# Optimization experiments

Hardware: AMD Instinct MI355X
Metric: run time of the kernel (lower is better)

The kernel has to match this reference:

```python
import jax, jax.numpy as jnp
import numpy as np

N_BATCH = 2; N_RAYS = 4096; S_COARSE = 32; S_FINE = 32
FEATURE_DIM = 32; BOX_WARP = 6.0; EPS = 1e-5

_PLANE_AXES = np.array([[[1, 0, 0], [0, 1, 0], [0, 0, 1]],
                        [[1, 0, 0], [0, 0, 1], [0, 1, 0]],
                        [[0, 0, 1], [0, 1, 0], [1, 0, 0]]], dtype=np.float32)
_INV_PLANES = np.linalg.inv(_PLANE_AXES)  # [3,3,3]


def _grid_sample(feat, coords):
    # feat [B,C,H,W], coords [B,M,2] in [-1,1] (x->W, y->H); bilinear, align_corners=False, zero padding
    B, C, H, W = feat.shape
    x = (coords[..., 0] + 1.0) * (W * 0.5) - 0.5
    y = (coords[..., 1] + 1.0) * (H * 0.5) - 0.5
    x0 = jnp.floor(x); y0 = jnp.floor(y)
    wx = x - x0; wy = y - y0
    x0i = x0.astype(jnp.int32); y0i = y0.astype(jnp.int32)

    def corner(fb, yi, xi):
        valid = ((xi >= 0) & (xi < W) & (yi >= 0) & (yi < H)).astype(fb.dtype)
        v = fb[:, jnp.clip(yi, 0, H - 1), jnp.clip(xi, 0, W - 1)]  # [C,M]
        return v * valid[None, :]

    def one(fb, x0b, y0b, wxb, wyb):
        x1b = x0b + 1; y1b = y0b + 1
        return (corner(fb, y0b, x0b) * (1 - wxb) * (1 - wyb)
                + corner(fb, y0b, x1b) * wxb * (1 - wyb)
                + corner(fb, y1b, x0b) * (1 - wxb) * wyb
                + corner(fb, y1b, x1b) * wxb * wyb)  # [C,M]

    return jax.vmap(one)(feat, x0i, y0i, wx, wy)  # [B,C,M]


def _sample_from_planes(planes, coords):
    # planes [N,3,C,H,W], coords [N,M,3] -> [N,3,M,C]
    N, n_planes, C, H, W = planes.shape
    M = coords.shape[1]
    c = coords * (2.0 / BOX_WARP)
    proj = jnp.einsum('nmc,pcd->npmd', c, jnp.asarray(_INV_PLANES))[..., :2]  # [N,3,M,2]
    out = _grid_sample(planes.reshape(N * n_planes, C, H, W), proj.reshape(N * n_planes, M, 2))
    return out.reshape(N, n_planes, C, M).transpose(0, 1, 3, 2)


def _decoder(feat, W1, b1, W2, b2):
    # OSGDecoder: Linear -> softplus -> Linear; rgb sigmoid-squashed, sigma raw
    h = jax.nn.softplus(feat @ W1 + b1)
    o = h @ W2 + b2
    rgb = jax.nn.sigmoid(o[..., 1:]) * (1 + 2 * 0.001) - 0.001
    sigma = o[..., 0:1]
    return rgb, sigma


def _run_model(planes, coords, W1, b1, W2, b2, beta):
    sf = _sample_from_planes(planes, coords).mean(axis=1)  # [N,M,C]
    rgb, raw_sigma = _decoder(sf, W1, b1, W2, b2)
    pred_sdf = raw_sigma
    # template SDF stand-in (external FLAME tex_feature net): sphere SDF
    tsdf = jnp.linalg.norm(coords, axis=-1, keepdims=True) - 0.5
    sigma = raw_sigma + tsdf
    density = jax.nn.sigmoid(-sigma / beta) / beta  # sdf_activation(-sigma)
    return rgb, density, pred_sdf


def _ray_march(colors, densities, depths):
    deltas = depths[:, :, 1:] - depths[:, :, :-1]
    c_mid = 0.5 * (colors[:, :, :-1] + colors[:, :, 1:])
    d_mid = 0.5 * (densities[:, :, :-1] + densities[:, :, 1:])
    z_mid = 0.5 * (depths[:, :, :-1] + depths[:, :, 1:])
    alpha = 1.0 - jnp.exp(-d_mid * deltas)
    shifted = jnp.concatenate([jnp.ones_like(alpha[:, :, :1]), 1.0 - alpha + 1e-10], axis=2)
    weights = alpha * jnp.cumprod(shifted, axis=2)[:, :, :-1]
    comp_rgb = jnp.sum(weights * c_mid, axis=2) * 2.0 - 1.0
    w_tot = jnp.sum(weights, axis=2)
    comp_depth = jnp.sum(weights * z_mid, axis=2) / w_tot
    comp_depth = jnp.nan_to_num(comp_depth, nan=jnp.inf)
    comp_depth = jnp.clip(comp_depth, depths.min(), depths.max())
    return comp_rgb, comp_depth, weights


def _sample_pdf(bins, weights, u):
    n_w = weights.shape[-1]
    w = weights + EPS
    pdf = w / jnp.sum(w, axis=-1, keepdims=True)
    cdf = jnp.cumsum(pdf, axis=-1)
    cdf = jnp.concatenate([jnp.zeros_like(cdf[:, :1]), cdf], axis=-1)
    inds = jax.vmap(lambda c, uu: jnp.searchsorted(c, uu, side='right'))(cdf, u)
    below = jnp.maximum(inds - 1, 0)
    above = jnp.minimum(inds, n_w)
    cdf0 = jnp.take_along_axis(cdf, below, axis=-1)
    cdf1 = jnp.take_along_axis(cdf, above, axis=-1)
    b0 = jnp.take_along_axis(bins, below, axis=-1)
    b1v = jnp.take_along_axis(bins, above, axis=-1)
    denom = cdf1 - cdf0
    denom = jnp.where(denom < EPS, 1.0, denom)
    return b0 + (u - cdf0) / denom * (b1v - b0)


def _sample_importance(z_vals, weights, u):
    B, R, S, _ = z_vals.shape
    z = z_vals.reshape(B * R, S)
    w = weights.reshape(B * R, -1)  # S-1
    # torch max_pool1d(k=2,s=1,pad=1) then avg_pool1d(k=2,s=1)
    neg = jnp.full_like(w[:, :1], -1e10)
    wp = jnp.concatenate([neg, w, neg], axis=-1)
    m = jnp.maximum(wp[:, :-1], wp[:, 1:])  # len S
    w_sm = 0.5 * (m[:, :-1] + m[:, 1:]) + 0.01  # len S-1
    z_mid = 0.5 * (z[:, :-1] + z[:, 1:])  # len S-1
    s = _sample_pdf(z_mid, w_sm[:, 1:-1], u)
    return jax.lax.stop_gradient(s.reshape(B, R, -1, 1))


def reference(planes, ray_origins, ray_directions, hit_min_depth, hit_max_depth, jitter, u_importance, W1, b1, W2, b2, sigmoid_beta, hit_mask):
    N, M, _ = ray_origins.shape
    beta = jnp.maximum(sigmoid_beta, 0.002)
    mask = hit_mask.astype(planes.dtype)[:, :, None, None]  # [N,M,1,1]
    hmin = jnp.where(mask == 0, hit_min_depth.min(), hit_min_depth)
    hmax = jnp.where(mask == 0, hit_max_depth.max(), hit_max_depth)
    base = jnp.linspace(0.0, 1.0, S_COARSE, dtype=planes.dtype).reshape(1, 1, S_COARSE, 1)
    span = hmax - hmin
    d_coarse = (base + jitter * span / S_COARSE) * span + hmin  # [N,M,S,1]

    def eval_points(depths):
        coords = ray_origins[:, :, None, :] + depths * ray_directions[:, :, None, :]
        S = depths.shape[2]
        rgb, dens, psdf = _run_model(planes, coords.reshape(N, M * S, 3), W1, b1, W2, b2, beta)
        # masked scatter-back into dense buffers == multiply by hit mask
        rgb = rgb.reshape(N, M, S, FEATURE_DIM) * mask
        dens = dens.reshape(N, M, S, 1) * mask
        return rgb, dens, psdf

    rgb_c, dens_c, psdf_c = eval_points(d_coarse)
    _, _, w_c = _ray_march(rgb_c, dens_c, d_coarse)
    d_fine = _sample_importance(d_coarse, w_c, u_importance)
    rgb_f, dens_f, psdf_f = eval_points(d_fine)

    all_d = jnp.concatenate([d_coarse, d_fine], axis=2)
    all_c = jnp.concatenate([rgb_c, rgb_f], axis=2)
    all_s = jnp.concatenate([dens_c, dens_f], axis=2)
    idx = jnp.argsort(all_d, axis=2)
    all_d = jnp.take_along_axis(all_d, idx, axis=2)
    all_c = jnp.take_along_axis(all_c, jnp.broadcast_to(idx, all_c.shape), axis=2)
    all_s = jnp.take_along_axis(all_s, jnp.broadcast_to(idx, all_s.shape), axis=2)

    rgb_final, depth_final, weights = _ray_march(all_c, all_s, all_d)
    all_pred_sdf = jnp.concatenate([psdf_c, psdf_f], axis=1)
    return rgb_final, depth_final, weights, all_pred_sdf


def setup_inputs():
    key = jax.random.key(0)
    ks = jax.random.split(key, 12)
    planes = jax.random.normal(ks[0], (N_BATCH, 3, 32, 256, 256), jnp.float32)
    ray_origins = 0.1 * jax.random.normal(ks[1], (N_BATCH, N_RAYS, 3), jnp.float32)
    rd = jax.random.normal(ks[2], (N_BATCH, N_RAYS, 3), jnp.float32)
    ray_directions = rd / jnp.linalg.norm(rd, axis=-1, keepdims=True)
    hit_min_depth = 0.8 + 0.4 * jax.random.uniform(ks[3], (N_BATCH, N_RAYS, 1, 1), jnp.float32)
    hit_max_depth = hit_min_depth + 0.5 + jax.random.uniform(ks[4], (N_BATCH, N_RAYS, 1, 1), jnp.float32)
    jitter = jax.random.uniform(ks[5], (N_BATCH, N_RAYS, S_COARSE, 1), jnp.float32)
    u_importance = jax.random.uniform(ks[6], (N_BATCH * N_RAYS, S_FINE), jnp.float32)
    W1 = 0.05 * jax.random.normal(ks[7], (32, 64), jnp.float32)
    b1 = jnp.zeros((64,), jnp.float32)
    W2 = 0.05 * jax.random.normal(ks[8], (64, 1 + FEATURE_DIM), jnp.float32)
    b2 = jnp.zeros((1 + FEATURE_DIM,), jnp.float32)
    sigmoid_beta = 0.1 * jnp.ones((1,), jnp.float32)
    hit_mask = jax.random.randint(ks[9], (N_BATCH, N_RAYS), 0, 2, jnp.int32)
    return {'planes': planes, 'ray_origins': ray_origins, 'ray_directions': ray_directions,
            'hit_min_depth': hit_min_depth, 'hit_max_depth': hit_max_depth, 'jitter': jitter,
            'u_importance': u_importance, 'W1': W1, 'b1': b1, 'W2': W2, 'b2': b2,
            'sigmoid_beta': sigmoid_beta, 'hit_mask': hit_mask}
```

## Files before the change

kernel.cpp:

```cpp
#include <hip/hip_runtime.h>
#include <hip/hip_bf16.h>
#include <math.h>
#include <stddef.h>

typedef unsigned int u32;
typedef unsigned short u16;
typedef unsigned long long u64;

#define NRAYS 8192
#define NSAMP 262144

__device__ __forceinline__ float fa(float a,float b){ return __fadd_rn(a,b); }
__device__ __forceinline__ float fs(float a,float b){ return __fsub_rn(a,b); }
__device__ __forceinline__ float fm(float a,float b){ return __fmul_rn(a,b); }
__device__ __forceinline__ float fdv(float a,float b){ return __fdiv_rn(a,b); }

__device__ __forceinline__ double exp_d(double x){
  const double LOG2E  = 1.4426950408889634074;
  const double LN2_HI = 6.93147180369123816490e-01;
  const double LN2_LO = 1.90821492927058770002e-10;
  double kd = rint(x * LOG2E);
  if (kd >  200.0) return INFINITY;
  if (kd < -200.0) return 0.0;
  int k = (int)kd;
  double r = fma(-kd, LN2_HI, x);
  r = fma(-kd, LN2_LO, r);
  double p = 1.0/39916800.0;
  p = fma(p, r, 1.0/3628800.0);
  p = fma(p, r, 1.0/362880.0);
  p = fma(p, r, 1.0/40320.0);
  p = fma(p, r, 1.0/5040.0);
  p = fma(p, r, 1.0/720.0);
  p = fma(p, r, 1.0/120.0);
  p = fma(p, r, 1.0/24.0);
  p = fma(p, r, 1.0/6.0);
  p = fma(p, r, 0.5);
  p = fma(p, r, 1.0);
  p = fma(p, r, 1.0);
  u64 sb = ((u64)(k + 1023)) << 52;
  return p * __longlong_as_double((long long)sb);
}
__device__ __forceinline__ float exf(float x){ return (float)exp_d((double)x); }
__device__ __forceinline__ float sigm(float x){
  if (x >= 0.f){ float e = exf(-x); return fdv(1.f, fa(1.f, e)); }
  float e = exf(x); return fdv(e, fa(1.f, e));
}
__device__ __forceinline__ float sigm_fast(float x){
  return 1.f/(1.f + __expf(-x));
}
__device__ __forceinline__ u16 f2b(float f){
  u32 x = __float_as_uint(f);
  return (u16)((x + 0x7fffu + ((x>>16)&1u)) >> 16);
}
__device__ __forceinline__ u32 fenc(float f){ u32 b=__float_as_uint(f); return (b&0x80000000u)? ~b : (b|0x80000000u); }
__device__ __forceinline__ float fdec(u32 k){ u32 b=(k&0x80000000u)? (k^0x80000000u) : ~k; return __uint_as_float(b); }

__global__ void k_init(const float* __restrict__ hmin, const float* __restrict__ hmax,
                       const float* __restrict__ W1, float* __restrict__ scal,
                       float* __restrict__ W1t){
  __shared__ float smn[256], smx[256];
  int t = threadIdx.x;
  float mn = 1e30f, mx = -1e30f;
  for (int i=t;i<NRAYS;i+=256){ mn=fminf(mn,hmin[i]); mx=fmaxf(mx,hmax[i]); }
  smn[t]=mn; smx[t]=mx; __syncthreads();
  for(int s=128;s>0;s>>=1){
    if(t<s){ smn[t]=fminf(smn[t],smn[t+s]); smx[t]=fmaxf(smx[t],smx[t+s]); }
    __syncthreads();
  }
  if(t==0){
    scal[0]=smn[0]; scal[1]=smx[0];
    ((u32*)scal)[2]=0xFFFFFFFFu;
    ((u32*)scal)[3]=0u;
  }
  for(int i=t;i<2048;i+=256){ int j=i>>5, c=i&31; W1t[i]=W1[c*64+j]; }
}

__global__ void __launch_bounds__(256) k_tr(const float* __restrict__ pl, float* __restrict__ pt){
  int t = blockIdx.x*256 + threadIdx.x;
  int x  = t & 255;
  int c4 = ((t>>8)&7)<<2;
  int y  = (t>>11)&255;
  int np = t>>19;
  const float* ip = pl + (((size_t)(np*32+c4))<<16) + (y<<8) + x;
  float4 o;
  o.x = ip[0];
  o.y = ip[65536];
  o.z = ip[131072];
  o.w = ip[196608];
  *reinterpret_cast<float4*>(pt + ((((size_t)(np<<8|y))<<8|x)<<5) + c4) = o;
}

template<int PHASE>
__global__ void __launch_bounds__(256) k_eval(
  const float* __restrict__ pt, const float* __restrict__ ro, const float* __restrict__ rd,
  const float* __restrict__ hmin, const float* __restrict__ hmax,
  const float* __restrict__ jitter, const int* __restrict__ hitmask,
  const float* __restrict__ W1t, const float* __restrict__ b1,
  const float* __restrict__ W2, const float* __restrict__ b2,
  const float* __restrict__ sb, float* __restrict__ scal,
  float* __restrict__ dep, float* __restrict__ dens_out, u16* __restrict__ rgb_out,
  float* __restrict__ out_psdf)
{
  int idx = blockIdx.x*256 + threadIdx.x;
  int ray = idx >> 5;
  int s   = idx & 31;
  int n   = ray >> 12;
  int msk = hitmask[ray];

  float d;
  if (PHASE==0){
    float hmn = msk ? hmin[ray] : scal[0];
    float hmx = msk ? hmax[ray] : scal[1];
    float span = fs(hmx, hmn);
    float jit  = jitter[idx];
    float base = (float)((double)s * (1.0/31.0));
    if (s==31) base = 1.0f;
    float t1 = fdv(fm(jit, span), 32.0f);
    d = fa(fm(fa(base, t1), span), hmn);
    dep[idx] = d;
    float dm=d, dM=d;
#pragma unroll
    for (int m=1;m<64;m<<=1){ dm=fminf(dm,__shfl_xor(dm,m)); dM=fmaxf(dM,__shfl_xor(dM,m)); }
    if ((threadIdx.x & 63)==0){
      atomicMin(((u32*)scal)+2, fenc(dm));
      atomicMax(((u32*)scal)+3, fenc(dM));
    }
  } else {
    d = dep[idx];
  }

  float ox=ro[ray*3+0], oy=ro[ray*3+1], oz=ro[ray*3+2];
  float dx=rd[ray*3+0], dy=rd[ray*3+1], dz=rd[ray*3+2];
  float px = fa(ox, fm(d,dx)), py = fa(oy, fm(d,dy)), pz = fa(oz, fm(d,dz));
  float nrm = __fsqrt_rn(fa(fa(fm(px,px),fm(py,py)),fm(pz,pz)));
  float tsdf = fs(nrm, 0.5f);
  const float sc2 = (float)(2.0/6.0);
  float cx=fm(px,sc2), cy=fm(py,sc2), cz=fm(pz,sc2);

  float feat[32];
#pragma unroll
  for(int c=0;c<32;c++) feat[c]=0.f;

#pragma unroll
  for (int p=0;p<3;p++){
    float u = (p==2)?cz:cx;
    float v = (p==1)?cz:cy;
    float fx = fs(fm(fa(u,1.f),128.f),0.5f);
    float fy = fs(fm(fa(v,1.f),128.f),0.5f);
    float x0f = floorf(fx), y0f = floorf(fy);
    float wx = fs(fx,x0f), wy = fs(fy,y0f);
    float ax0 = fs(1.f,wx), ax1 = wx, ay0 = fs(1.f,wy), ay1 = wy;
    int x0, y0;
    {
      x0 = (x0f >= 2.1e9f) ? 2147483647 : ((x0f <= -2.1e9f) ? (-2147483647-1) : (int)x0f);
      y0 = (y0f >= 2.1e9f) ? 2147483647 : ((y0f <= -2.1e9f) ? (-2147483647-1) : (int)y0f);
    }
    int x1=x0+1, y1=y0+1;
    bool vx0 = (x0>=0 && x0<256), vx1 = (x1>=0 && x1<256);
    bool vy0 = (y0>=0 && y0<256), vy1 = (y1>=0 && y1<256);
    bool ok00 = vx0&&vy0, ok01 = vx1&&vy0, ok10 = vx0&&vy1, ok11 = vx1&&vy1;
    int cx0=min(max(x0,0),255), cx1=min(max(x1,0),255);
    int cy0=min(max(y0,0),255), cy1=min(max(y1,0),255);
    int npl = n*3+p;
    size_t pb = ((size_t)npl)<<16;
    const float4* t00 = (const float4*)(pt + ((pb + (cy0<<8) + cx0)<<5));
    const float4* t01 = (const float4*)(pt + ((pb + (cy0<<8) + cx1)<<5));
    const float4* t10 = (const float4*)(pt + ((pb + (cy1<<8) + cx0)<<5));
    const float4* t11 = (const float4*)(pt + ((pb + (cy1<<8) + cx1)<<5));
#pragma unroll
    for(int q=0;q<8;q++){
      float4 v00 = t00[q], v01 = t01[q], v10 = t10[q], v11 = t11[q];
      float e0,e1,e2,e3, t_;
#define CORNER_SUM(FLD, OUTI) \
      e0 = ok00 ? v00.FLD : 0.f; e1 = ok01 ? v01.FLD : 0.f; \
      e2 = ok10 ? v10.FLD : 0.f; e3 = ok11 ? v11.FLD : 0.f; \
      t_ = fa(fa(fa(fm(fm(e0,ax0),ay0), fm(fm(e1,ax1),ay0)), fm(fm(e2,ax0),ay1)), fm(fm(e3,ax1),ay1)); \
      feat[q*4+OUTI] = fa(feat[q*4+OUTI], t_);
      CORNER_SUM(x,0) CORNER_SUM(y,1) CORNER_SUM(z,2) CORNER_SUM(w,3)
#undef CORNER_SUM
    }
  }
#pragma unroll
  for(int c=0;c<32;c++) feat[c] = fdv(feat[c], 3.0f);

  float o[33];
#pragma unroll
  for(int k=0;k<33;k++) o[k]=0.f;
#pragma unroll 2
  for(int j=0;j<64;j++){
    float a = 0.f;
#pragma unroll
    for(int c=0;c<32;c++) a = fmaf(feat[c], W1t[j*32+c], a);
    a = fa(a, b1[j]);
    float h = fa(fmaxf(a,0.f), __logf(fa(1.f, __expf(-fabsf(a)))));
#pragma unroll
    for(int k=0;k<33;k++) o[k] = fmaf(h, W2[j*33+k], o[k]);
  }
#pragma unroll
  for(int k=0;k<33;k++) o[k] = fa(o[k], b2[k]);

  float beta = fmaxf(sb[0], 0.002f);
  float raw = o[0];
  out_psdf[((size_t)n<<18) + ((size_t)PHASE<<17) + (size_t)(ray&4095)*32 + s] = raw;
  float sg = fa(raw, tsdf);
  float dens = msk ? fdv(sigm(fdv(-sg, beta)), beta) : 0.f;
  dens_out[idx]=dens;

  u16 rv[32];
#pragma unroll
  for(int c=0;c<32;c++){
    float r = msk ? fs(fm(sigm_fast(o[c+1]), 1.002f), 0.001f) : 0.f;
    rv[c]=f2b(r);
  }
  uint4* op = (uint4*)(rgb_out + (size_t)idx*32);
#pragma unroll
  for(int q=0;q<4;q++){
    uint4 w;
    w.x = (u32)rv[q*8+0] | ((u32)rv[q*8+1]<<16);
    w.y = (u32)rv[q*8+2] | ((u32)rv[q*8+3]<<16);
    w.z = (u32)rv[q*8+4] | ((u32)rv[q*8+5]<<16);
    w.w = (u32)rv[q*8+6] | ((u32)rv[q*8+7]<<16);
    op[q]=w;
  }
}

__global__ void __launch_bounds__(64) k_imp(
  const float* __restrict__ dc, const float* __restrict__ dens,
  const float* __restrict__ u_imp, float* __restrict__ df, float* __restrict__ scal)
{
  __shared__ float scdf[64][30];
  __shared__ float szm [64][30];
  int tid = threadIdx.x;
  int ray = blockIdx.x*64 + tid;
  float w[31];
  float dprev = dc[ray*32+0];
  float sprev = dens[ray*32+0];
  float T = 1.f;
#pragma unroll
  for(int i=0;i<31;i++){
    float dn = dc[ray*32+i+1];
    float sn = dens[ray*32+i+1];
    if (i<30) szm[tid][i] = fm(0.5f, fa(dprev,dn));
    float delta = fs(dn,dprev);
    float dm = fm(0.5f, fa(sprev,sn));
    float al = fs(1.f, exf(-fm(dm,delta)));
    w[i] = fm(al,T);
    T = fm(T, fa(fs(1.f,al), 1e-10f));
    dprev=dn; sprev=sn;
  }
  float pdfw[29];
#pragma unroll
  for(int i=0;i<29;i++){
    float m1 = fmaxf(w[i],w[i+1]), m2 = fmaxf(w[i+1],w[i+2]);
    pdfw[i] = fa(fa(fm(0.5f, fa(m1,m2)), 0.01f), 1e-5f);
  }
  float sum;
  {
    float r[8];
#pragma unroll
    for(int j=0;j<8;j++) r[j]=pdfw[j];
#pragma unroll
    for(int j=0;j<8;j++) r[j]=fa(r[j],pdfw[8+j]);
#pragma unroll
    for(int j=0;j<8;j++) r[j]=fa(r[j],pdfw[16+j]);
    sum = fa(fa(fa(r[0],r[1]),fa(r[2],r[3])), fa(fa(r[4],r[5]),fa(r[6],r[7])));
#pragma unroll
    for(int i=24;i<29;i++) sum = fa(sum, pdfw[i]);
  }
  {
    float cacc = 0.f;
    scdf[tid][0] = 0.f;
#pragma unroll
    for(int i=1;i<30;i++){
      cacc = fa(cacc, fdv(pdfw[i-1], sum));
      scdf[tid][i] = cacc;
    }
  }

  float fmn=1e30f, fmx=-1e30f;
  for(int k=0;k<32;k++){
    float u = u_imp[ray*32+k];
    int lo=0, hi=30;
    while(lo<hi){
      int mid=(lo+hi)>>1;
      if (scdf[tid][mid] <= u) lo = mid+1; else hi = mid;
    }
    int ind = lo;
    int below = ind-1;
    int above = (ind>29)?29:ind;
    float cdf0 = scdf[tid][below];
    float cdf1 = scdf[tid][above];
    float b0   = szm [tid][below];
    float b1v  = szm [tid][above];
    float den = fs(cdf1,cdf0);
    if((double)den < 1e-5) den = 1.f;
    float sres = fa(b0, fm(fdv(fs(u,cdf0),den), fs(b1v,b0)));
    df[ray*32+k]=sres;
    fmn=fminf(fmn,sres); fmx=fmaxf(fmx,sres);
  }
#pragma unroll
  for(int m=1;m<64;m<<=1){ fmn=fminf(fmn,__shfl_xor(fmn,m)); fmx=fmaxf(fmx,__shfl_xor(fmx,m)); }
  if(tid==0){
    atomicMin(((u32*)scal)+2, fenc(fmn));
    atomicMax(((u32*)scal)+3, fenc(fmx));
  }
}

__global__ void __launch_bounds__(256) k_final(
  const float* __restrict__ dc, const float* __restrict__ df,
  const float* __restrict__ densc, const float* __restrict__ densf,
  const u16* __restrict__ rgbc, const u16* __restrict__ rgbf,
  const float* __restrict__ scal,
  float* __restrict__ out_rgb, float* __restrict__ out_depth, float* __restrict__ out_w)
{
  __shared__ float ssd[4][64];
  __shared__ float ssn[4][64];
  __shared__ int   sp [4][64];
  __shared__ float swv[4][64];
  __shared__ float swz[4][64];
  int wid = threadIdx.x>>6, lane = threadIdx.x&63;
  int ray = blockIdx.x*4 + wid;

  float myd = (lane<32)? dc[ray*32+lane]    : df[ray*32+lane-32];
  float myn = (lane<32)? densc[ray*32+lane] : densf[ray*32+lane-32];
  ssd[wid][lane]=myd; __syncthreads();
  int rk=0;
#pragma unroll 8
  for(int j=0;j<64;j++){
    float dj = ssd[wid][j];
    rk += (dj<myd || (dj==myd && j<lane)) ? 1:0;
  }
  __syncthreads();
  ssd[wid][rk]=myd; ssn[wid][rk]=myn; sp[wid][rk]=lane;
  __syncthreads();

  float T=1.f, accr=0.f;
  int j0 = sp[wid][0];
  float cprev = 0.f;
  if (lane<32){
    const u16* cb = (j0<32)? (rgbc+((size_t)ray*32+j0)*32) : (rgbf+((size_t)ray*32+(j0-32))*32);
    cprev = __uint_as_float(((u32)cb[lane])<<16);
  }
  float d0 = ssd[wid][0], n0 = ssn[wid][0];
  for(int s2=0;s2<63;s2++){
    float d1 = ssd[wid][s2+1], n1 = ssn[wid][s2+1];
    float delta = fs(d1,d0);
    float dm = fm(0.5f, fa(n0,n1));
    float al = fs(1.f, exf(-fm(dm,delta)));
    float wv = fm(al,T);
    T = fm(T, fa(fs(1.f,al), 1e-10f));
    if (lane==s2){ swv[wid][s2]=wv; swz[wid][s2]=fm(wv, fm(0.5f, fa(d0,d1))); }
    int j1 = sp[wid][s2+1];
    float cnext = 0.f;
    if (lane<32){
      const u16* cb = (j1<32)? (rgbc+((size_t)ray*32+j1)*32) : (rgbf+((size_t)ray*32+(j1-32))*32);
      cnext = __uint_as_float(((u32)cb[lane])<<16);
    }
    accr = fa(accr, fm(wv, fm(0.5f, fa(cprev,cnext))));
    cprev=cnext; d0=d1; n0=n1;
  }
  __syncthreads();
  if(lane<63) out_w[(size_t)ray*63+lane]=swv[wid][lane];
  if(lane<32) out_rgb[(size_t)ray*32+lane]=fs(fm(accr,2.f),1.f);
  if(lane==0){
    float wsum, zsum;
    {
      float r[8], rz[8];
#pragma unroll
      for(int j=0;j<8;j++){ r[j]=swv[wid][j]; rz[j]=swz[wid][j]; }
      for(int i=8;i<56;i+=8)
#pragma unroll
        for(int j=0;j<8;j++){ r[j]=fa(r[j],swv[wid][i+j]); rz[j]=fa(rz[j],swz[wid][i+j]); }
      wsum = fa(fa(fa(r[0],r[1]),fa(r[2],r[3])), fa(fa(r[4],r[5]),fa(r[6],r[7])));
      zsum = fa(fa(fa(rz[0],rz[1]),fa(rz[2],rz[3])), fa(fa(rz[4],rz[5]),fa(rz[6],rz[7])));
      for(int i=56;i<63;i++){ wsum=fa(wsum,swv[wid][i]); zsum=fa(zsum,swz[wid][i]); }
    }
    float depv = fdv(zsum, wsum);
    if (isnan(depv)) depv = INFINITY;
    float lo = fdec(((const u32*)scal)[2]);
    float hi = fdec(((const u32*)scal)[3]);
    depv = fminf(fmaxf(depv,lo),hi);
    out_depth[ray]=depv;
  }
}

extern "C" void kernel_launch(void* const* d_in, const int* in_sizes, int n_in,
                              void* d_out, int out_size, void* d_ws, size_t ws_size,
                              hipStream_t stream) {
  const float* planes = (const float*)d_in[0];
  const float* ro     = (const float*)d_in[1];
  const float* rdp    = (const float*)d_in[2];
  const float* hmin   = (const float*)d_in[3];
  const float* hmax   = (const float*)d_in[4];
  const float* jitter = (const float*)d_in[5];
  const float* uimp   = (const float*)d_in[6];
  const float* W1     = (const float*)d_in[7];
  const float* b1     = (const float*)d_in[8];
  const float* W2     = (const float*)d_in[9];
  const float* b2     = (const float*)d_in[10];
  const float* sb     = (const float*)d_in[11];
  const int*   hmk    = (const int*)d_in[12];
  float* out = (float*)d_out;
  char* ws = (char*)d_ws;

  size_t off=0;
  auto alloc=[&](size_t bytes){ size_t o=off; off=(off+bytes+255)&~(size_t)255; return o; };
  float* scal = (float*)(ws+alloc(64));
  float* W1t  = (float*)(ws+alloc(2048*4));
  float* pt   = (float*)(ws+alloc((size_t)12582912*4));
  float* dco  = (float*)(ws+alloc((size_t)NSAMP*4));
  float* dfi  = (float*)(ws+alloc((size_t)NSAMP*4));
  float* dnc  = (float*)(ws+alloc((size_t)NSAMP*4));
  float* dnf  = (float*)(ws+alloc((size_t)NSAMP*4));
  u16*   rgc  = (u16*)  (ws+alloc((size_t)NSAMP*32*2));
  u16*   rgf  = (u16*)  (ws+alloc((size_t)NSAMP*32*2));
  (void)in_sizes; (void)n_in; (void)out_size; (void)ws_size;

  float* out_rgb  = out;
  float* out_dep  = out + 262144;
  float* out_w    = out + 270336;
  float* out_psdf = out + 786432;

  k_init<<<dim3(1),dim3(256),0,stream>>>(hmin,hmax,W1,scal,W1t);
  k_tr<<<dim3(12288),dim3(256),0,stream>>>(planes, pt);
  k_eval<0><<<dim3(1024),dim3(256),0,stream>>>(pt,ro,rdp,hmin,hmax,jitter,hmk,W1t,b1,W2,b2,sb,scal,dco,dnc,rgc,out_psdf);
  k_imp<<<dim3(128),dim3(64),0,stream>>>(dco,dnc,uimp,dfi,scal);
  k_eval<1><<<dim3(1024),dim3(256),0,stream>>>(pt,ro,rdp,hmin,hmax,jitter,hmk,W1t,b1,W2,b2,sb,scal,dfi,dnf,rgf,out_psdf);
  k_final<<<dim3(2048),dim3(256),0,stream>>>(dco,dfi,dnc,dnf,rgc,rgf,scal,out_rgb,out_dep,out_w);
}
```

Measured before the change: 457.5 us.

## Cooperatively gather plane features with 8 lanes per sample via shared memory

The triplane bilinear gather is restructured so that 8 lanes cooperate on each sample point, each loading one float4 channel chunk from the four corners. Results are staged in shared memory and then read back per thread for the MLP. This makes the gather loads coalesced across lanes, where previously each thread fetched 32 contiguous floats on its own. In exchange, sample position is recomputed per chunk, the kernel gains about 33 KB of LDS and a block barrier, and the per-sample gather loop is serialized over 8 rounds.

```diff
diff --git a/kernel.cpp b/kernel.cpp
--- a/kernel.cpp
+++ b/kernel.cpp
@@ -101,7 +101,12 @@
   float* __restrict__ dep, float* __restrict__ dens_out, u16* __restrict__ rgb_out,
   float* __restrict__ out_psdf)
 {
-  int idx = blockIdx.x*256 + threadIdx.x;
+  __shared__ float sfeat[4][64][33];
+  int tid = threadIdx.x;
+  int wid = tid>>6, lane = tid&63;
+  int blockbase = blockIdx.x*256;
+  int wavebase  = blockbase + (wid<<6);
+  int idx = blockbase + tid;
   int ray = idx >> 5;
   int s   = idx & 31;
   int n   = ray >> 12;
@@ -121,7 +126,7 @@
     float dm=d, dM=d;
 #pragma unroll
     for (int m=1;m<64;m<<=1){ dm=fminf(dm,__shfl_xor(dm,m)); dM=fmaxf(dM,__shfl_xor(dM,m)); }
-    if ((threadIdx.x & 63)==0){
+    if ((tid & 63)==0){
       atomicMin(((u32*)scal)+2, fenc(dm));
       atomicMax(((u32*)scal)+3, fenc(dM));
     }
@@ -129,59 +134,93 @@
     d = dep[idx];
   }
 
-  float ox=ro[ray*3+0], oy=ro[ray*3+1], oz=ro[ray*3+2];
-  float dx=rd[ray*3+0], dy=rd[ray*3+1], dz=rd[ray*3+2];
-  float px = fa(ox, fm(d,dx)), py = fa(oy, fm(d,dy)), pz = fa(oz, fm(d,dz));
-  float nrm = __fsqrt_rn(fa(fa(fm(px,px),fm(py,py)),fm(pz,pz)));
-  float tsdf = fs(nrm, 0.5f);
+  float tsdf;
+  {
+    float ox=ro[ray*3+0], oy=ro[ray*3+1], oz=ro[ray*3+2];
+    float dx=rd[ray*3+0], dy=rd[ray*3+1], dz=rd[ray*3+2];
+    float px = fa(ox, fm(d,dx)), py = fa(oy, fm(d,dy)), pz = fa(oz, fm(d,dz));
+    float nrm = __fsqrt_rn(fa(fa(fm(px,px),fm(py,py)),fm(pz,pz)));
+    tsdf = fs(nrm, 0.5f);
+  }
+
   const float sc2 = (float)(2.0/6.0);
-  float cx=fm(px,sc2), cy=fm(py,sc2), cz=fm(pz,sc2);
-
-  float feat[32];
-#pragma unroll
-  for(int c=0;c<32;c++) feat[c]=0.f;
-
-#pragma unroll
-  for (int p=0;p<3;p++){
-    float u = (p==2)?cz:cx;
-    float v = (p==1)?cz:cy;
-    float fx = fs(fm(fa(u,1.f),128.f),0.5f);
-    float fy = fs(fm(fa(v,1.f),128.f),0.5f);
-    float x0f = floorf(fx), y0f = floorf(fy);
-    float wx = fs(fx,x0f), wy = fs(fy,y0f);
-    float ax0 = fs(1.f,wx), ax1 = wx, ay0 = fs(1.f,wy), ay1 = wy;
-    int x0, y0;
-    {
-      x0 = (x0f >= 2.1e9f) ? 2147483647 : ((x0f <= -2.1e9f) ? (-2147483647-1) : (int)x0f);
-      y0 = (y0f >= 2.1e9f) ? 2147483647 : ((y0f <= -2.1e9f) ? (-2147483647-1) : (int)y0f);
-    }
-    int x1=x0+1, y1=y0+1;
-    bool vx0 = (x0>=0 && x0<256), vx1 = (x1>=0 && x1<256);
-    bool vy0 = (y0>=0 && y0<256), vy1 = (y1>=0 && y1<256);
-    bool ok00 = vx0&&vy0, ok01 = vx1&&vy0, ok10 = vx0&&vy1, ok11 = vx1&&vy1;
-    int cx0=min(max(x0,0),255), cx1=min(max(x1,0),255);
-    int cy0=min(max(y0,0),255), cy1=min(max(y1,0),255);
-    int npl = n*3+p;
-    size_t pb = ((size_t)npl)<<16;
-    const float4* t00 = (const float4*)(pt + ((pb + (cy0<<8) + cx0)<<5));
-    const float4* t01 = (const float4*)(pt + ((pb + (cy0<<8) + cx1)<<5));
-    const float4* t10 = (const float4*)(pt + ((pb + (cy1<<8) + cx0)<<5));
-    const float4* t11 = (const float4*)(pt + ((pb + (cy1<<8) + cx1)<<5));
-#pragma unroll
-    for(int q=0;q<8;q++){
-      float4 v00 = t00[q], v01 = t01[q], v10 = t10[q], v11 = t11[q];
+  int pg = lane >> 3;
+  int q  = lane & 7;
+#pragma unroll 1
+  for (int r=0;r<8;r++){
+    int p2   = wavebase + r*8 + pg;
+    int ray2 = p2 >> 5;
+    int s2   = p2 & 31;
+    int n2   = ray2 >> 12;
+    float d2;
+    if (PHASE==0){
+      int msk2 = hitmask[ray2];
+      float hmn = msk2 ? hmin[ray2] : scal[0];
+      float hmx = msk2 ? hmax[ray2] : scal[1];
+      float span = fs(hmx, hmn);
+      float jit  = jitter[p2];
+      float base = (float)((double)s2 * (1.0/31.0));
+      if (s2==31) base = 1.0f;
+      float t1 = fdv(fm(jit, span), 32.0f);
+      d2 = fa(fm(fa(base, t1), span), hmn);
+    } else {
+      d2 = dep[p2];
+    }
+    float ox=ro[ray2*3+0], oy=ro[ray2*3+1], oz=ro[ray2*3+2];
+    float dx=rd[ray2*3+0], dy=rd[ray2*3+1], dz=rd[ray2*3+2];
+    float px = fa(ox, fm(d2,dx)), py = fa(oy, fm(d2,dy)), pz = fa(oz, fm(d2,dz));
+    float cx=fm(px,sc2), cy=fm(py,sc2), cz=fm(pz,sc2);
+
+    float fchunk[4];
+#pragma unroll
+    for(int i=0;i<4;i++) fchunk[i]=0.f;
+
+#pragma unroll
+    for (int p=0;p<3;p++){
+      float u = (p==2)?cz:cx;
+      float v = (p==1)?cz:cy;
+      float fx = fs(fm(fa(u,1.f),128.f),0.5f);
+      float fy = fs(fm(fa(v,1.f),128.f),0.5f);
+      float x0f = floorf(fx), y0f = floorf(fy);
+      float wx = fs(fx,x0f), wy = fs(fy,y0f);
+      float ax0 = fs(1.f,wx), ax1 = wx, ay0 = fs(1.f,wy), ay1 = wy;
+      int x0, y0;
+      {
+        x0 = (x0f >= 2.1e9f) ? 2147483647 : ((x0f <= -2.1e9f) ? (-2147483647-1) : (int)x0f);
+        y0 = (y0f >= 2.1e9f) ? 2147483647 : ((y0f <= -2.1e9f) ? (-2147483647-1) : (int)y0f);
+      }
+      int x1=x0+1, y1=y0+1;
+      bool vx0 = (x0>=0 && x0<256), vx1 = (x1>=0 && x1<256);
+      bool vy0 = (y0>=0 && y0<256), vy1 = (y1>=0 && y1<256);
+      bool ok00 = vx0&&vy0, ok01 = vx1&&vy0, ok10 = vx0&&vy1, ok11 = vx1&&vy1;
+      int cx0=min(max(x0,0),255), cx1=min(max(x1,0),255);
+      int cy0=min(max(y0,0),255), cy1=min(max(y1,0),255);
+      size_t pb = ((size_t)(n2*3+p))<<16;
+      int qo = q<<2;
+      const float4* t00 = (const float4*)(pt + ((pb + (cy0<<8) + cx0)<<5) + qo);
+      const float4* t01 = (const float4*)(pt + ((pb + (cy0<<8) + cx1)<<5) + qo);
+      const float4* t10 = (const float4*)(pt + ((pb + (cy1<<8) + cx0)<<5) + qo);
+      const float4* t11 = (const float4*)(pt + ((pb + (cy1<<8) + cx1)<<5) + qo);
+      float4 v00 = *t00, v01 = *t01, v10 = *t10, v11 = *t11;
       float e0,e1,e2,e3, t_;
 #define CORNER_SUM(FLD, OUTI) \
       e0 = ok00 ? v00.FLD : 0.f; e1 = ok01 ? v01.FLD : 0.f; \
       e2 = ok10 ? v10.FLD : 0.f; e3 = ok11 ? v11.FLD : 0.f; \
       t_ = fa(fa(fa(fm(fm(e0,ax0),ay0), fm(fm(e1,ax1),ay0)), fm(fm(e2,ax0),ay1)), fm(fm(e3,ax1),ay1)); \
-      feat[q*4+OUTI] = fa(feat[q*4+OUTI], t_);
+      fchunk[OUTI] = fa(fchunk[OUTI], t_);
       CORNER_SUM(x,0) CORNER_SUM(y,1) CORNER_SUM(z,2) CORNER_SUM(w,3)
 #undef CORNER_SUM
     }
-  }
-#pragma unroll
-  for(int c=0;c<32;c++) feat[c] = fdv(feat[c], 3.0f);
+    int pidx = r*8 + pg;
+#pragma unroll
+    for(int i=0;i<4;i++)
+      sfeat[wid][pidx][q*4+i] = fdv(fchunk[i], 3.0f);
+  }
+  __syncthreads();
+
+  float feat[32];
+#pragma unroll
+  for(int c=0;c<32;c++) feat[c] = sfeat[wid][lane][c];
 
   float o[33];
 #pragma unroll
@@ -214,13 +253,13 @@
   }
   uint4* op = (uint4*)(rgb_out + (size_t)idx*32);
 #pragma unroll
-  for(int q=0;q<4;q++){
+  for(int q2=0;q2<4;q2++){
     uint4 w;
-    w.x = (u32)rv[q*8+0] | ((u32)rv[q*8+1]<<16);
-    w.y = (u32)rv[q*8+2] | ((u32)rv[q*8+3]<<16);
-    w.z = (u32)rv[q*8+4] | ((u32)rv[q*8+5]<<16);
-    w.w = (u32)rv[q*8+6] | ((u32)rv[q*8+7]<<16);
-    op[q]=w;
+    w.x = (u32)rv[q2*8+0] | ((u32)rv[q2*8+1]<<16);
+    w.y = (u32)rv[q2*8+2] | ((u32)rv[q2*8+3]<<16);
+    w.z = (u32)rv[q2*8+4] | ((u32)rv[q2*8+5]<<16);
+    w.w = (u32)rv[q2*8+6] | ((u32)rv[q2*8+7]<<16);
+    op[q2]=w;
   }
 }
 
```

Result: faster. 424.5 us (-7.2%).
